# Kernel optimization log

Hardware: AMD Instinct MI355X
Metric: run time of the kernel (lower is better)

Reference implementation:

```python
import jax, jax.numpy as jnp
import numpy as np

P_SCALAR = 40.0
NEG_INF = -1e9


def setup_inputs() -> dict:
    key = jax.random.key(0)
    ks = jax.random.split(key, 6)
    B, Dk, Dv, T, H, W = 2, 128, 512, 2, 64, 64
    qkey = jax.random.normal(ks[0], (B, Dk, H, W), dtype=jnp.float32)
    qval = jax.random.normal(ks[1], (B, Dv, H, W), dtype=jnp.float32)
    mkey = jax.random.normal(ks[2], (B, Dk, T, H, W), dtype=jnp.float32)
    mval = jax.random.normal(ks[3], (B, Dv, T, H, W), dtype=jnp.float32)
    qmask = jax.random.bernoulli(ks[4], 0.5, (B, 1, H, W))
    mmask = jax.random.bernoulli(ks[5], 0.5, (B, 1, T, H, W))
    return {"qkey": qkey, "qval": qval, "qmask": qmask,
            "mkey": mkey, "mval": mval, "mmask": mmask}


def reference(qkey, qval, qmask, mkey, mval, mmask):
    # Faithful vectorized version of maskRead: for each batch, attention from
    # masked query pixels over masked memory pixels, scatter back into zeros.
    # Boolean-gather + softmax over gathered rows == full softmax with masked
    # logits set to -inf (rows outside mmask get zero probability).
    B, Dk, H, W = qkey.shape
    Dv = qval.shape[1]
    qk = qkey.reshape(B, Dk, H * W)            # [B, Dk, Nq]
    mk = mkey.reshape(B, Dk, -1)               # [B, Dk, Nm]
    mv = mval.reshape(B, Dv, -1)               # [B, Dv, Nm]
    qm = qmask.reshape(B, H * W)               # [B, Nq]
    mm = mmask.reshape(B, -1)                  # [B, Nm]

    # p[b, m, q] = <mk[b,:,m], qk[b,:,q]> * p_scalar, softmax over m
    p = jnp.einsum('bdm,bdq->bmq', mk, qk) * P_SCALAR
    p = jnp.where(mm[:, :, None], p, NEG_INF)
    p = jax.nn.softmax(p, axis=1)              # [B, Nm, Nq]

    read = jnp.einsum('bvm,bmq->bvq', mv, p)   # [B, Dv, Nq]

    # zero out query pixels outside qmask; skip batches with empty masks
    valid = qm[:, None, :] & mm.any(axis=1)[:, None, None] & qm.any(axis=1)[:, None, None]
    qread = jnp.where(valid, read, 0.0)
    return qread.reshape(B, Dv, H, W)
```

## Files before the change

### kernel.cpp

```cpp
#include <hip/hip_runtime.h>
#include <hip/hip_fp16.h>

#define NQ 4096
#define NM 8192
#define DK 128
#define DV 512
#define BATCH 2
#define NT (NM / 64)
#define KTS 8192
#define VTILE 16384

typedef __attribute__((ext_vector_type(8))) short short8;
typedef __attribute__((ext_vector_type(4))) float f32x4;
typedef unsigned short ushort_t;

#define MF(A_, B_, C_) __builtin_amdgcn_mfma_f32_16x16x32_bf16(A_, B_, C_, 0, 0, 0)

static __device__ __forceinline__ unsigned short f2bf(float x) {
    union { float f; unsigned int u; } c; c.f = x;
    unsigned int u = c.u;
    return (unsigned short)((u + 0x7FFFu + ((u >> 16) & 1u)) >> 16);
}
static __device__ __forceinline__ float bf2f(unsigned short h) {
    union { unsigned int u; float f; } c; c.u = ((unsigned int)h) << 16;
    return c.f;
}
static __device__ __forceinline__ ushort_t f2h(float x) {
    __half h = __float2half(x);
    return *(ushort_t*)&h;
}
static __device__ __forceinline__ float h2f(ushort_t u) {
    __half h = *(__half*)&u;
    return __half2float(h);
}

static __device__ __forceinline__ size_t vaddr(int b, int pos, int dv) {
    const int mt = pos >> 6, m64 = pos & 63;
    const int dvh = dv >> 8, rr = dv & 255;
    return (((size_t)(b * NT + mt) * 2 + dvh) * VTILE)
         + (rr >> 6) * 4096 + ((rr >> 4) & 3) * 1024
         + (m64 >> 5) * 512
         + ((((m64 >> 4) & 1) * 2 + ((m64 >> 3) & 1)) * 128)
         + (rr & 15) * 8 + (m64 & 7);
}

#define LOADK(AH, AL, itn_) do {                                              \
    const size_t ktb_ = kbase + (size_t)(itn_) * KTS;                         \
    _Pragma("unroll")                                                         \
    for (int ks_ = 0; ks_ < 4; ++ks_) {                                       \
        AH[ks_] = *(const short8*)(kh0 + ktb_ + ks_ * 512);                   \
        AL[ks_] = *(const short8*)(kl0 + ktb_ + ks_ * 512);                   \
    }                                                                         \
} while (0)

__global__ __launch_bounds__(1024) void scan_kernel(
    const int* __restrict__ qmask, const int* __restrict__ mmask,
    int* __restrict__ cidx, int* __restrict__ cpos,
    int* __restrict__ cnts, int* __restrict__ qflags) {
    const int b = blockIdx.x;
    const int t = threadIdx.x;
    const int lane = t & 63;
    const int w = t >> 6;
    __shared__ int wsum[16];
    __shared__ int qsh;

    const int* mp = mmask + b * NM;
    const int base = t * 8;
    int val[8];
#pragma unroll
    for (int i = 0; i < 8; ++i) val[i] = (mp[base + i] != 0);
    int c0 = 0;
#pragma unroll
    for (int i = 0; i < 8; ++i) c0 += val[i];

    int c = c0;
#pragma unroll
    for (int off = 1; off < 64; off <<= 1) {
        int n = __shfl_up(c, off, 64);
        if (lane >= off) c += n;
    }
    if (lane == 63) wsum[w] = c;
    if (t == 0) qsh = 0;
    __syncthreads();
    if (t == 0) {
        int s = 0;
#pragma unroll
        for (int i = 0; i < 16; ++i) { s += wsum[i]; wsum[i] = s; }
    }
    __syncthreads();
    const int wbase = (w == 0) ? 0 : wsum[w - 1];
    int run = wbase + (c - c0);
#pragma unroll
    for (int i = 0; i < 8; ++i) {
        int m = base + i;
        cpos[b * NM + m] = run;
        if (val[i]) { cidx[b * NM + run] = m; ++run; }
    }

    int qa = 0;
    for (int i = t; i < NQ; i += 1024) qa |= (qmask[b * NQ + i] != 0);
    if (qa) atomicOr(&qsh, 1);
    __syncthreads();
    if (t == 0) { cnts[b] = wsum[15]; qflags[b] = qsh; }
}

__global__ __launch_bounds__(256) void prep_qk_kernel(
    const float* __restrict__ qkey, const float* __restrict__ mkey,
    const int* __restrict__ mmask, const int* __restrict__ cpos,
    ushort_t* __restrict__ Qhi, ushort_t* __restrict__ Qlo,
    ushort_t* __restrict__ Khi, ushort_t* __restrict__ Klo) {
    __shared__ float t32[32][33];
    const int g = blockIdx.x;

    if (g < 1024) {
        const int bx = g & 127, by = (g >> 7) & 3, b = g >> 9;
        const int d0 = by * 32, n0 = bx * 32;
        for (int l = threadIdx.x; l < 1024; l += 256) {
            int r = l >> 5, c = l & 31;
            t32[r][c] = qkey[((size_t)b * DK + d0 + r) * NQ + n0 + c];
        }
        __syncthreads();
        for (int l = threadIdx.x; l < 1024; l += 256) {
            int r = l >> 5, c = l & 31;
            float f = t32[c][r];
            unsigned short h = f2bf(f);
            unsigned short lw = f2bf(f - bf2f(h));
            size_t off = ((size_t)b * NQ + n0 + r) * DK + d0 + c;
            Qhi[off] = h;
            Qlo[off] = lw;
        }
        return;
    }
    const int h0 = g - 1024;
    const int bx = h0 & 255, by = (h0 >> 8) & 3, b = h0 >> 10;
    const int d0 = by * 32, n0 = bx * 32;
    for (int l = threadIdx.x; l < 1024; l += 256) {
        int r = l >> 5, c = l & 31;
        t32[r][c] = mkey[((size_t)b * DK + d0 + r) * NM + n0 + c];
    }
    __syncthreads();
    for (int l = threadIdx.x; l < 1024; l += 256) {
        int r = l >> 5, c = l & 31;
        int m = n0 + r;
        if (mmask[b * NM + m] != 0) {
            int pos = cpos[b * NM + m];
            float f = t32[c][r];
            unsigned short hh = f2bf(f);
            unsigned short lw = f2bf(f - bf2f(hh));
            int d = d0 + c;
            size_t off = ((size_t)(b * NT + (pos >> 6))) * KTS
                       + ((pos >> 4) & 3) * 2048 + (d >> 5) * 512
                       + ((d >> 3) & 3) * 128 + (pos & 15) * 8 + (d & 7);
            Khi[off] = hh;
            Klo[off] = lw;
        }
    }
}

__global__ __launch_bounds__(256) void prep_v_kernel(
    const float* __restrict__ src, const int* __restrict__ mmask,
    const int* __restrict__ cpos, const int* __restrict__ cnts,
    ushort_t* __restrict__ dst) {
    const int b = blockIdx.z;
    const int dv0 = blockIdx.x * 8;
    if (blockIdx.y == 8) {
        const int cnt = cnts[b];
        const int pend = ((cnt + 63) >> 6) * 64;
        const int dv = dv0 + (threadIdx.x >> 5);
        for (int p = cnt + (threadIdx.x & 31); p < pend; p += 32)
            dst[vaddr(b, p, dv)] = 0;
        return;
    }
    const int m = blockIdx.y * 1024 + threadIdx.x * 4;
    const int4 mm = *(const int4*)(mmask + b * NM + m);
    const int4 cp = *(const int4*)(cpos + b * NM + m);
#pragma unroll
    for (int i = 0; i < 8; ++i) {
        const int dv = dv0 + i;
        const float4 v = *(const float4*)(src + ((size_t)b * DV + dv) * NM + m);
        if (mm.x) dst[vaddr(b, cp.x, dv)] = f2bf(v.x);
        if (mm.y) dst[vaddr(b, cp.y, dv)] = f2bf(v.y);
        if (mm.z) dst[vaddr(b, cp.z, dv)] = f2bf(v.z);
        if (mm.w) dst[vaddr(b, cp.w, dv)] = f2bf(v.w);
    }
}

__global__ __launch_bounds__(256, 3) void stats_kernel(
    const ushort_t* __restrict__ Qhi, const ushort_t* __restrict__ Khi,
    const int* __restrict__ cnts, float* __restrict__ mpart) {
    const int t = threadIdx.x;
    const int lane = t & 63;
    const int w = t >> 6;
    const int quad = lane >> 4;
    const int col = lane & 15;
    const int bid = blockIdx.x;
    const int part = bid & 3;
    const int b = (bid >> 2) & 1;
    const int qb = (bid >> 3) * 64;

    const int cnt = cnts[b];
    const int nit = (cnt + 63) >> 6;
    const int it0 = (nit * part) >> 2;
    const int it1 = (nit * (part + 1)) >> 2;

    __shared__ float red_m[4][64];

    short8 qfh[4][4];
    {
        const ushort_t* qhp = Qhi + ((size_t)b * NQ + qb) * DK;
#pragma unroll
        for (int qt = 0; qt < 4; ++qt)
#pragma unroll
            for (int ks = 0; ks < 4; ++ks)
                qfh[qt][ks] = *(const short8*)(qhp + (size_t)(qt * 16 + col) * DK + ks * 32 + quad * 8);
    }

    const f32x4 zero4 = {0.f, 0.f, 0.f, 0.f};
    float mloc[4] = {-3.0e38f, -3.0e38f, -3.0e38f, -3.0e38f};
    const ushort_t* kh0 = Khi + w * 2048 + lane * 8;
    const size_t kbase = (size_t)(b * NT) * KTS;

#define LOADKH(A_, itn_) do {                                                 \
    const size_t ktb_ = kbase + (size_t)(itn_) * KTS;                         \
    _Pragma("unroll")                                                         \
    for (int ks_ = 0; ks_ < 4; ++ks_)                                         \
        A_[ks_] = *(const short8*)(kh0 + ktb_ + ks_ * 512);                   \
} while (0)

#define STPH(CK, NK, it_, itn_) do {                                          \
    LOADKH(NK, itn_);                                                         \
    f32x4 aS[4];                                                              \
    _Pragma("unroll")                                                         \
    for (int qt = 0; qt < 4; ++qt) aS[qt] = zero4;                            \
    _Pragma("unroll")                                                         \
    for (int ks = 0; ks < 4; ++ks)                                            \
        _Pragma("unroll")                                                     \
        for (int qt = 0; qt < 4; ++qt)                                        \
            aS[qt] = MF(CK[ks], qfh[qt][ks], aS[qt]);                         \
    const int mrow_ = (it_) * 64 + w * 16 + quad * 4;                         \
    _Pragma("unroll")                                                         \
    for (int r = 0; r < 4; ++r) {                                             \
        if (mrow_ + r < cnt) {                                                \
            _Pragma("unroll")                                                 \
            for (int qt = 0; qt < 4; ++qt)                                    \
                mloc[qt] = fmaxf(mloc[qt], aS[qt][r] * 40.0f);                \
        }                                                                     \
    }                                                                         \
} while (0)

    short8 kA[4], kB[4];
    int it = it0;
    if (it < it1) {
        LOADKH(kA, it);
        int itn;
        while (true) {
            itn = (it + 1 < it1) ? it + 1 : it;
            STPH(kA, kB, it, itn);
            if (++it >= it1) break;
            itn = (it + 1 < it1) ? it + 1 : it;
            STPH(kB, kA, it, itn);
            if (++it >= it1) break;
        }
    }
#undef STPH
#undef LOADKH

#pragma unroll
    for (int qt = 0; qt < 4; ++qt) {
        float m = mloc[qt];
        m = fmaxf(m, __shfl_xor(m, 16, 64));
        m = fmaxf(m, __shfl_xor(m, 32, 64));
        if (lane < 16) red_m[w][qt * 16 + col] = m;
    }
    __syncthreads();
    if (t < 64) {
        float M = -3.0e38f;
#pragma unroll
        for (int ww = 0; ww < 4; ++ww) M = fmaxf(M, red_m[ww][t]);
        mpart[((size_t)(b * 4 + part)) * NQ + qb + t] = M;
    }
}

__global__ __launch_bounds__(256, 3) void pv_kernel(
    const ushort_t* __restrict__ Qhi, const ushort_t* __restrict__ Qlo,
    const ushort_t* __restrict__ Khi, const ushort_t* __restrict__ Klo,
    const ushort_t* __restrict__ Vimg, const int* __restrict__ cnts,
    const float* __restrict__ mpart, ushort_t* __restrict__ out0,
    ushort_t* __restrict__ out1, ushort_t* __restrict__ out2,
    float* __restrict__ lsum) {
    const int t = threadIdx.x;
    const int lane = t & 63;
    const int w = t >> 6;
    const int quad = lane >> 4;
    const int col = lane & 15;
    const int bid = blockIdx.x;
    const int b = bid & 1;
    const int dvh = (bid >> 1) & 1;
    const int r3 = bid >> 2;
    const int chunk = r3 % 3;
    const int qb = (r3 / 3) * 64;

    const int cnt = cnts[b];
    const int nit = (cnt + 63) >> 6;
    const int it0 = (nit * chunk) / 3;
    const int it1 = (nit * (chunk + 1)) / 3;

    __shared__ __align__(16) ushort_t Q_s[2][4][4][512];
    __shared__ __align__(16) ushort_t P_s[2][64][68];

    float gm[4];
#pragma unroll
    for (int qt = 0; qt < 4; ++qt) {
        float M = -3.0e38f;
#pragma unroll
        for (int c = 0; c < 4; ++c)
            M = fmaxf(M, mpart[((size_t)(b * 4 + c)) * NQ + qb + qt * 16 + col]);
        gm[qt] = M + 8.0f;
    }

    {
        const int r = t >> 2, ks4 = t & 3;
        const int qt_ = r >> 4, col_ = r & 15;
        const ushort_t* qhp = Qhi + ((size_t)b * NQ + qb + r) * DK + ks4 * 32;
        const ushort_t* qlp = Qlo + ((size_t)b * NQ + qb + r) * DK + ks4 * 32;
#pragma unroll
        for (int qd = 0; qd < 4; ++qd) {
            *(short8*)&Q_s[0][qt_][ks4][qd * 128 + col_ * 8] = *(const short8*)(qhp + qd * 8);
            *(short8*)&Q_s[1][qt_][ks4][qd * 128 + col_ * 8] = *(const short8*)(qlp + qd * 8);
        }
    }
    __syncthreads();

    const ushort_t* kh0 = Khi + w * 2048 + lane * 8;
    const ushort_t* kl0 = Klo + w * 2048 + lane * 8;
    const size_t kbase = (size_t)(b * NT) * KTS;
    const ushort_t* vl0 = Vimg + ((size_t)(b * NT) * 2 + dvh) * VTILE
                        + w * 4096 + lane * 8;

    const f32x4 zero4 = {0.f, 0.f, 0.f, 0.f};
    const short8 vones = {(short)0x3F80, (short)0x3F80, (short)0x3F80,
                          (short)0x3F80, (short)0x3F80, (short)0x3F80,
                          (short)0x3F80, (short)0x3F80};
    const bool doL = (dvh == 0) && (w == 0);
    f32x4 accO[4][4];
#pragma unroll
    for (int vt = 0; vt < 4; ++vt)
#pragma unroll
        for (int qt = 0; qt < 4; ++qt) accO[vt][qt] = zero4;
    f32x4 accL[4];
#pragma unroll
    for (int qt = 0; qt < 4; ++qt) accL[qt] = zero4;

    for (int it = it0; it < it1; ++it) {
        const int pb = (it - it0) & 1;
        short8 kh[4], kl[4];
        LOADK(kh, kl, it);
        f32x4 aS[4];
#pragma unroll
        for (int qt = 0; qt < 4; ++qt) aS[qt] = zero4;
        __builtin_amdgcn_s_setprio(1);
#pragma unroll
        for (int qt = 0; qt < 4; ++qt) {
#pragma unroll
            for (int ks = 0; ks < 4; ++ks) {
                const short8 qh = *(const short8*)&Q_s[0][qt][ks][lane * 8];
                const short8 ql = *(const short8*)&Q_s[1][qt][ks][lane * 8];
                aS[qt] = MF(kh[ks], qh, aS[qt]);
                aS[qt] = MF(kh[ks], ql, aS[qt]);
                aS[qt] = MF(kl[ks], qh, aS[qt]);
            }
        }
        __builtin_amdgcn_s_setprio(0);
        const ushort_t* vp = vl0 + (size_t)it * (2 * VTILE);
        short8 vf[4][2];
#pragma unroll
        for (int vt = 0; vt < 4; ++vt) {
            vf[vt][0] = *(const short8*)(vp + vt * 1024);
            vf[vt][1] = *(const short8*)(vp + vt * 1024 + 512);
        }
        const int mrow = it * 64 + w * 16 + quad * 4;
#pragma unroll
        for (int qt = 0; qt < 4; ++qt) {
            float p[4];
#pragma unroll
            for (int r = 0; r < 4; ++r)
                p[r] = (mrow + r < cnt) ? __expf(aS[qt][r] * 40.0f - gm[qt]) : 0.0f;
            ushort4 pk;
            pk.x = f2bf(p[0]); pk.y = f2bf(p[1]);
            pk.z = f2bf(p[2]); pk.w = f2bf(p[3]);
            *(ushort4*)&P_s[pb][qt * 16 + col][w * 16 + quad * 4] = pk;
        }
        asm volatile("s_waitcnt lgkmcnt(0)" ::: "memory");
        __builtin_amdgcn_s_barrier();
        __builtin_amdgcn_sched_barrier(0);
        __builtin_amdgcn_s_setprio(1);
#pragma unroll
        for (int k2 = 0; k2 < 2; ++k2) {
            short8 pq[4];
#pragma unroll
            for (int qt = 0; qt < 4; ++qt)
                pq[qt] = *(const short8*)&P_s[pb][qt * 16 + col][k2 * 32 + quad * 8];
#pragma unroll
            for (int vt = 0; vt < 4; ++vt)
#pragma unroll
                for (int qt = 0; qt < 4; ++qt)
                    accO[vt][qt] = MF(vf[vt][k2], pq[qt], accO[vt][qt]);
            if (doL) {
#pragma unroll
                for (int qt = 0; qt < 4; ++qt)
                    accL[qt] = MF(vones, pq[qt], accL[qt]);
            }
        }
        __builtin_amdgcn_s_setprio(0);
    }

    ushort_t* pbase = (chunk == 0) ? out0 : ((chunk == 1) ? out1 : out2);
#pragma unroll
    for (int qt = 0; qt < 4; ++qt) {
        const int q = qb + qt * 16 + col;
#pragma unroll
        for (int vt = 0; vt < 4; ++vt)
#pragma unroll
            for (int r = 0; r < 4; ++r) {
                int dv = dvh * 256 + w * 64 + vt * 16 + quad * 4 + r;
                pbase[((size_t)b * DV + dv) * NQ + q] = f2h(accO[vt][qt][r]);
            }
    }
    if (doL && lane < 16) {
#pragma unroll
        for (int qt = 0; qt < 4; ++qt)
            lsum[((size_t)(b * 3 + chunk)) * NQ + qb + qt * 16 + col] = accL[qt][0];
    }
}

__global__ __launch_bounds__(256) void combine_kernel(
    const ushort_t* __restrict__ p0, const ushort_t* __restrict__ p1,
    const ushort_t* __restrict__ p2, const float* __restrict__ lsum,
    const int* __restrict__ cnts, const int* __restrict__ qflags,
    const int* __restrict__ qmask, float* __restrict__ out) {
    const size_t i = ((size_t)blockIdx.x * 256 + threadIdx.x) * 4;
    const int b = (int)(i >> 21);
    const int q = (int)(i & (NQ - 1));
    ushort4 a4 = *(const ushort4*)(p0 + i);
    ushort4 c4 = *(const ushort4*)(p1 + i);
    ushort4 d4 = *(const ushort4*)(p2 + i);
    f32x4 l0 = *(const f32x4*)(lsum + (size_t)(b * 3) * NQ + q);
    f32x4 l1 = *(const f32x4*)(lsum + (size_t)(b * 3 + 1) * NQ + q);
    f32x4 l2 = *(const f32x4*)(lsum + (size_t)(b * 3 + 2) * NQ + q);
    const int4 qm = *(const int4*)(qmask + b * NQ + q);
    const bool bv = (qflags[b] != 0) && (cnts[b] > 0);
    f32x4 r;
    float lv;
    lv = l0[0] + l1[0] + l2[0];
    r[0] = (bv && qm.x && lv > 0.f) ? (h2f(a4.x) + h2f(c4.x) + h2f(d4.x)) / lv : 0.f;
    lv = l0[1] + l1[1] + l2[1];
    r[1] = (bv && qm.y && lv > 0.f) ? (h2f(a4.y) + h2f(c4.y) + h2f(d4.y)) / lv : 0.f;
    lv = l0[2] + l1[2] + l2[2];
    r[2] = (bv && qm.z && lv > 0.f) ? (h2f(a4.z) + h2f(c4.z) + h2f(d4.z)) / lv : 0.f;
    lv = l0[3] + l1[3] + l2[3];
    r[3] = (bv && qm.w && lv > 0.f) ? (h2f(a4.w) + h2f(c4.w) + h2f(d4.w)) / lv : 0.f;
    *(f32x4*)(out + i) = r;
}

extern "C" void kernel_launch(void* const* d_in, const int* in_sizes, int n_in,
                              void* d_out, int out_size, void* d_ws, size_t ws_size,
                              hipStream_t stream) {
    const float* qkey  = (const float*)d_in[0];
    const int*   qmask = (const int*)d_in[2];
    const float* mkey  = (const float*)d_in[3];
    const float* mval  = (const float*)d_in[4];
    const int*   mmask = (const int*)d_in[5];
    float* out = (float*)d_out;

    char* ws = (char*)d_ws;
    size_t off = 0;
    const size_t QS  = (size_t)BATCH * NQ * DK * 2;
    const size_t KS2 = (size_t)BATCH * NM * DK * 2;
    const size_t VS  = (size_t)BATCH * NT * 2 * VTILE * 2;
    const size_t OS2 = (size_t)BATCH * DV * NQ * 2;
    ushort_t* Qhi = (ushort_t*)(ws + off); off += QS;
    ushort_t* Qlo = (ushort_t*)(ws + off); off += QS;
    ushort_t* Khi = (ushort_t*)(ws + off); off += KS2;
    ushort_t* Klo = (ushort_t*)(ws + off); off += KS2;
    ushort_t* Vc  = (ushort_t*)(ws + off); off += VS;
    ushort_t* part0 = (ushort_t*)(ws + off); off += OS2;
    ushort_t* part1 = (ushort_t*)(ws + off); off += OS2;
    ushort_t* part2 = (ushort_t*)(ws + off); off += OS2;
    float* mpart  = (float*)(ws + off); off += (size_t)BATCH * 4 * NQ * 4;
    float* lsum   = (float*)(ws + off); off += (size_t)BATCH * 3 * NQ * 4;
    int* cidx     = (int*)(ws + off); off += (size_t)BATCH * NM * 4;
    int* cpos     = (int*)(ws + off); off += (size_t)BATCH * NM * 4;
    int* cnts     = (int*)(ws + off); off += 64;
    int* qflags   = (int*)(ws + off); off += 64;

    scan_kernel<<<BATCH, 1024, 0, stream>>>(qmask, mmask, cidx, cpos, cnts, qflags);

    prep_qk_kernel<<<3072, 256, 0, stream>>>(
        qkey, mkey, mmask, cpos, Qhi, Qlo, Khi, Klo);

    dim3 gv(DV / 8, 9, BATCH);
    prep_v_kernel<<<gv, 256, 0, stream>>>(mval, mmask, cpos, cnts, Vc);

    stats_kernel<<<(NQ / 64) * 8, 256, 0, stream>>>(Qhi, Khi, cnts, mpart);

    pv_kernel<<<(NQ / 64) * 12, 256, 0, stream>>>(
        Qhi, Qlo, Khi, Klo, Vc, cnts, mpart, part0, part1, part2, lsum);

    combine_kernel<<<(int)((size_t)BATCH * DV * NQ / 1024), 256, 0, stream>>>(
        part0, part1, part2, lsum, cnts, qflags, qmask, out);
}
```

Measured before the change: 221.6 us.

## Software-pipeline PV loop, compute row sums on VALU, fuse prep kernels

Restructures the pv_kernel main loop into a two-stage software pipeline. The QK^T MFMAs for tile it overlap the PV MFMAs for tile it-1, and K and V fragments are double-buffered in registers and prefetched one iteration ahead. Softmax row sums are now accumulated from the bf16-rounded P values on the VALU with a shuffle and LDS reduction, which removes the extra MFMA against a ones vector. The QK and V prep kernels are merged into one launch to cut launch overhead. Occupancy is lowered to 2 blocks per SM to make room for the extra registers, so latency hiding between waves may suffer.

After: 386.9 us. 74.6% more time.

```diff
diff --git a/kernel.cpp b/kernel.cpp
--- a/kernel.cpp
+++ b/kernel.cpp
@@ -50,6 +50,15 @@
     for (int ks_ = 0; ks_ < 4; ++ks_) {                                       \
         AH[ks_] = *(const short8*)(kh0 + ktb_ + ks_ * 512);                   \
         AL[ks_] = *(const short8*)(kl0 + ktb_ + ks_ * 512);                   \
+    }                                                                         \
+} while (0)
+
+#define LOADV(VB_, it_) do {                                                  \
+    const ushort_t* vp_ = vl0 + (size_t)(it_) * (2 * VTILE);                  \
+    _Pragma("unroll")                                                         \
+    for (int vt_ = 0; vt_ < 4; ++vt_) {                                       \
+        VB_[vt_][0] = *(const short8*)(vp_ + vt_ * 1024);                     \
+        VB_[vt_][1] = *(const short8*)(vp_ + vt_ * 1024 + 512);               \
     }                                                                         \
 } while (0)
 
@@ -104,11 +113,13 @@
     if (t == 0) { cnts[b] = wsum[15]; qflags[b] = qsh; }
 }
 
-__global__ __launch_bounds__(256) void prep_qk_kernel(
+__global__ __launch_bounds__(256) void prep_all_kernel(
     const float* __restrict__ qkey, const float* __restrict__ mkey,
-    const int* __restrict__ mmask, const int* __restrict__ cpos,
+    const float* __restrict__ mval, const int* __restrict__ mmask,
+    const int* __restrict__ cpos, const int* __restrict__ cnts,
     ushort_t* __restrict__ Qhi, ushort_t* __restrict__ Qlo,
-    ushort_t* __restrict__ Khi, ushort_t* __restrict__ Klo) {
+    ushort_t* __restrict__ Khi, ushort_t* __restrict__ Klo,
+    ushort_t* __restrict__ Vc) {
     __shared__ float t32[32][33];
     const int g = blockIdx.x;
 
@@ -131,57 +142,57 @@
         }
         return;
     }
-    const int h0 = g - 1024;
-    const int bx = h0 & 255, by = (h0 >> 8) & 3, b = h0 >> 10;
-    const int d0 = by * 32, n0 = bx * 32;
-    for (int l = threadIdx.x; l < 1024; l += 256) {
-        int r = l >> 5, c = l & 31;
-        t32[r][c] = mkey[((size_t)b * DK + d0 + r) * NM + n0 + c];
-    }
-    __syncthreads();
-    for (int l = threadIdx.x; l < 1024; l += 256) {
-        int r = l >> 5, c = l & 31;
-        int m = n0 + r;
-        if (mmask[b * NM + m] != 0) {
-            int pos = cpos[b * NM + m];
-            float f = t32[c][r];
-            unsigned short hh = f2bf(f);
-            unsigned short lw = f2bf(f - bf2f(hh));
-            int d = d0 + c;
-            size_t off = ((size_t)(b * NT + (pos >> 6))) * KTS
-                       + ((pos >> 4) & 3) * 2048 + (d >> 5) * 512
-                       + ((d >> 3) & 3) * 128 + (pos & 15) * 8 + (d & 7);
-            Khi[off] = hh;
-            Klo[off] = lw;
-        }
-    }
-}
-
-__global__ __launch_bounds__(256) void prep_v_kernel(
-    const float* __restrict__ src, const int* __restrict__ mmask,
-    const int* __restrict__ cpos, const int* __restrict__ cnts,
-    ushort_t* __restrict__ dst) {
-    const int b = blockIdx.z;
-    const int dv0 = blockIdx.x * 8;
-    if (blockIdx.y == 8) {
+    if (g < 3072) {
+        const int h0 = g - 1024;
+        const int bx = h0 & 255, by = (h0 >> 8) & 3, b = h0 >> 10;
+        const int d0 = by * 32, n0 = bx * 32;
+        for (int l = threadIdx.x; l < 1024; l += 256) {
+            int r = l >> 5, c = l & 31;
+            t32[r][c] = mkey[((size_t)b * DK + d0 + r) * NM + n0 + c];
+        }
+        __syncthreads();
+        for (int l = threadIdx.x; l < 1024; l += 256) {
+            int r = l >> 5, c = l & 31;
+            int m = n0 + r;
+            if (mmask[b * NM + m] != 0) {
+                int pos = cpos[b * NM + m];
+                float f = t32[c][r];
+                unsigned short hh = f2bf(f);
+                unsigned short lw = f2bf(f - bf2f(hh));
+                int d = d0 + c;
+                size_t off = ((size_t)(b * NT + (pos >> 6))) * KTS
+                           + ((pos >> 4) & 3) * 2048 + (d >> 5) * 512
+                           + ((d >> 3) & 3) * 128 + (pos & 15) * 8 + (d & 7);
+                Khi[off] = hh;
+                Klo[off] = lw;
+            }
+        }
+        return;
+    }
+    const int h0 = g - 3072;
+    const int bx = h0 & 63;
+    const int by = (h0 >> 6) % 9;
+    const int b = h0 / 576;
+    const int dv0 = bx * 8;
+    if (by == 8) {
         const int cnt = cnts[b];
         const int pend = ((cnt + 63) >> 6) * 64;
         const int dv = dv0 + (threadIdx.x >> 5);
         for (int p = cnt + (threadIdx.x & 31); p < pend; p += 32)
-            dst[vaddr(b, p, dv)] = 0;
+            Vc[vaddr(b, p, dv)] = 0;
         return;
     }
-    const int m = blockIdx.y * 1024 + threadIdx.x * 4;
+    const int m = by * 1024 + threadIdx.x * 4;
     const int4 mm = *(const int4*)(mmask + b * NM + m);
     const int4 cp = *(const int4*)(cpos + b * NM + m);
 #pragma unroll
     for (int i = 0; i < 8; ++i) {
         const int dv = dv0 + i;
-        const float4 v = *(const float4*)(src + ((size_t)b * DV + dv) * NM + m);
-        if (mm.x) dst[vaddr(b, cp.x, dv)] = f2bf(v.x);
-        if (mm.y) dst[vaddr(b, cp.y, dv)] = f2bf(v.y);
-        if (mm.z) dst[vaddr(b, cp.z, dv)] = f2bf(v.z);
-        if (mm.w) dst[vaddr(b, cp.w, dv)] = f2bf(v.w);
+        const float4 v = *(const float4*)(mval + ((size_t)b * DV + dv) * NM + m);
+        if (mm.x) Vc[vaddr(b, cp.x, dv)] = f2bf(v.x);
+        if (mm.y) Vc[vaddr(b, cp.y, dv)] = f2bf(v.y);
+        if (mm.z) Vc[vaddr(b, cp.z, dv)] = f2bf(v.z);
+        if (mm.w) Vc[vaddr(b, cp.w, dv)] = f2bf(v.w);
     }
 }
 
@@ -281,7 +292,7 @@
     }
 }
 
-__global__ __launch_bounds__(256, 3) void pv_kernel(
+__global__ __launch_bounds__(256, 2) void pv_kernel(
     const ushort_t* __restrict__ Qhi, const ushort_t* __restrict__ Qlo,
     const ushort_t* __restrict__ Khi, const ushort_t* __restrict__ Klo,
     const ushort_t* __restrict__ Vimg, const int* __restrict__ cnts,
@@ -307,6 +318,7 @@
 
     __shared__ __align__(16) ushort_t Q_s[2][4][4][512];
     __shared__ __align__(16) ushort_t P_s[2][64][68];
+    __shared__ float red_l[4][64];
 
     float gm[4];
 #pragma unroll
@@ -338,81 +350,110 @@
                         + w * 4096 + lane * 8;
 
     const f32x4 zero4 = {0.f, 0.f, 0.f, 0.f};
-    const short8 vones = {(short)0x3F80, (short)0x3F80, (short)0x3F80,
-                          (short)0x3F80, (short)0x3F80, (short)0x3F80,
-                          (short)0x3F80, (short)0x3F80};
-    const bool doL = (dvh == 0) && (w == 0);
     f32x4 accO[4][4];
 #pragma unroll
     for (int vt = 0; vt < 4; ++vt)
 #pragma unroll
         for (int qt = 0; qt < 4; ++qt) accO[vt][qt] = zero4;
-    f32x4 accL[4];
-#pragma unroll
-    for (int qt = 0; qt < 4; ++qt) accL[qt] = zero4;
-
-    for (int it = it0; it < it1; ++it) {
-        const int pb = (it - it0) & 1;
-        short8 kh[4], kl[4];
-        LOADK(kh, kl, it);
-        f32x4 aS[4];
-#pragma unroll
-        for (int qt = 0; qt < 4; ++qt) aS[qt] = zero4;
-        __builtin_amdgcn_s_setprio(1);
-#pragma unroll
-        for (int qt = 0; qt < 4; ++qt) {
-#pragma unroll
-            for (int ks = 0; ks < 4; ++ks) {
-                const short8 qh = *(const short8*)&Q_s[0][qt][ks][lane * 8];
-                const short8 ql = *(const short8*)&Q_s[1][qt][ks][lane * 8];
-                aS[qt] = MF(kh[ks], qh, aS[qt]);
-                aS[qt] = MF(kh[ks], ql, aS[qt]);
-                aS[qt] = MF(kl[ks], qh, aS[qt]);
-            }
-        }
-        __builtin_amdgcn_s_setprio(0);
-        const ushort_t* vp = vl0 + (size_t)it * (2 * VTILE);
-        short8 vf[4][2];
-#pragma unroll
-        for (int vt = 0; vt < 4; ++vt) {
-            vf[vt][0] = *(const short8*)(vp + vt * 1024);
-            vf[vt][1] = *(const short8*)(vp + vt * 1024 + 512);
-        }
-        const int mrow = it * 64 + w * 16 + quad * 4;
-#pragma unroll
-        for (int qt = 0; qt < 4; ++qt) {
-            float p[4];
-#pragma unroll
-            for (int r = 0; r < 4; ++r)
-                p[r] = (mrow + r < cnt) ? __expf(aS[qt][r] * 40.0f - gm[qt]) : 0.0f;
-            ushort4 pk;
-            pk.x = f2bf(p[0]); pk.y = f2bf(p[1]);
-            pk.z = f2bf(p[2]); pk.w = f2bf(p[3]);
-            *(ushort4*)&P_s[pb][qt * 16 + col][w * 16 + quad * 4] = pk;
+    float lacc[4] = {0.f, 0.f, 0.f, 0.f};
+
+#define QKBLK(KH_, KL_) do {                                                  \
+    __builtin_amdgcn_s_setprio(1);                                            \
+    _Pragma("unroll")                                                         \
+    for (int qt = 0; qt < 4; ++qt) {                                          \
+        _Pragma("unroll")                                                     \
+        for (int ks = 0; ks < 4; ++ks) {                                      \
+            const short8 qh = *(const short8*)&Q_s[0][qt][ks][lane * 8];      \
+            const short8 ql = *(const short8*)&Q_s[1][qt][ks][lane * 8];      \
+            aS[qt] = MF(KH_[ks], qh, aS[qt]);                                 \
+            aS[qt] = MF(KH_[ks], ql, aS[qt]);                                 \
+            aS[qt] = MF(KL_[ks], qh, aS[qt]);                                 \
+        }                                                                     \
+    }                                                                         \
+    __builtin_amdgcn_s_setprio(0);                                            \
+} while (0)
+
+#define PSTORE(PW_, it_) do {                                                 \
+    const int mrow_ = (it_) * 64 + w * 16 + quad * 4;                         \
+    _Pragma("unroll")                                                         \
+    for (int qt = 0; qt < 4; ++qt) {                                          \
+        float p_[4];                                                          \
+        _Pragma("unroll")                                                     \
+        for (int r = 0; r < 4; ++r)                                           \
+            p_[r] = (mrow_ + r < cnt) ? __expf(aS[qt][r] * 40.0f - gm[qt]) : 0.0f; \
+        ushort4 pk_;                                                          \
+        pk_.x = f2bf(p_[0]); pk_.y = f2bf(p_[1]);                             \
+        pk_.z = f2bf(p_[2]); pk_.w = f2bf(p_[3]);                             \
+        *(ushort4*)&P_s[PW_][qt * 16 + col][w * 16 + quad * 4] = pk_;         \
+        lacc[qt] += bf2f(pk_.x) + bf2f(pk_.y) + bf2f(pk_.z) + bf2f(pk_.w);    \
+    }                                                                         \
+} while (0)
+
+#define PVBLK(VP_, PBR_) do {                                                 \
+    short8 pq_[2][4];                                                         \
+    _Pragma("unroll")                                                         \
+    for (int k2 = 0; k2 < 2; ++k2)                                            \
+        _Pragma("unroll")                                                     \
+        for (int qt = 0; qt < 4; ++qt)                                        \
+            pq_[k2][qt] = *(const short8*)&P_s[PBR_][qt * 16 + col][k2 * 32 + quad * 8]; \
+    __builtin_amdgcn_s_setprio(1);                                            \
+    _Pragma("unroll")                                                         \
+    for (int k2 = 0; k2 < 2; ++k2)                                            \
+        _Pragma("unroll")                                                     \
+        for (int vt = 0; vt < 4; ++vt)                                        \
+            _Pragma("unroll")                                                 \
+            for (int qt = 0; qt < 4; ++qt)                                    \
+                accO[vt][qt] = MF(VP_[vt][k2], pq_[k2][qt], accO[vt][qt]);    \
+    __builtin_amdgcn_s_setprio(0);                                            \
+} while (0)
+
+#define PHASE(VP, VN, KC, KN, PBR, PBW, it_) do {                             \
+    LOADV(VN, it_);                                                           \
+    f32x4 aS[4];                                                              \
+    _Pragma("unroll")                                                         \
+    for (int qt = 0; qt < 4; ++qt) aS[qt] = zero4;                            \
+    QKBLK(KC##h, KC##l);                                                      \
+    { int itn_ = ((it_) + 1 < it1) ? (it_) + 1 : (it_);                       \
+      LOADK(KN##h, KN##l, itn_); }                                            \
+    PVBLK(VP, PBR);                                                           \
+    PSTORE(PBW, it_);                                                         \
+    asm volatile("s_waitcnt lgkmcnt(0)" ::: "memory");                        \
+    __builtin_amdgcn_s_barrier();                                             \
+    __builtin_amdgcn_sched_barrier(0);                                        \
+} while (0)
+
+    short8 kAh[4], kAl[4], kBh[4], kBl[4];
+    short8 vA[4][2], vB[4][2];
+    int it = it0;
+    if (it < it1) {
+        LOADV(vA, it);
+        LOADK(kAh, kAl, it);
+        {
+            f32x4 aS[4];
+#pragma unroll
+            for (int qt = 0; qt < 4; ++qt) aS[qt] = zero4;
+            QKBLK(kAh, kAl);
+            { int itn_ = (it + 1 < it1) ? it + 1 : it; LOADK(kBh, kBl, itn_); }
+            PSTORE(0, it);
         }
         asm volatile("s_waitcnt lgkmcnt(0)" ::: "memory");
         __builtin_amdgcn_s_barrier();
         __builtin_amdgcn_sched_barrier(0);
-        __builtin_amdgcn_s_setprio(1);
-#pragma unroll
-        for (int k2 = 0; k2 < 2; ++k2) {
-            short8 pq[4];
-#pragma unroll
-            for (int qt = 0; qt < 4; ++qt)
-                pq[qt] = *(const short8*)&P_s[pb][qt * 16 + col][k2 * 32 + quad * 8];
-#pragma unroll
-            for (int vt = 0; vt < 4; ++vt)
-#pragma unroll
-                for (int qt = 0; qt < 4; ++qt)
-                    accO[vt][qt] = MF(vf[vt][k2], pq[qt], accO[vt][qt]);
-            if (doL) {
-#pragma unroll
-                for (int qt = 0; qt < 4; ++qt)
-                    accL[qt] = MF(vones, pq[qt], accL[qt]);
-            }
-        }
-        __builtin_amdgcn_s_setprio(0);
-    }
+        ++it;
+        while (it < it1) {
+            PHASE(vA, vB, kB, kA, 0, 1, it);
+            if (++it >= it1) break;
+            PHASE(vB, vA, kA, kB, 1, 0, it);
+            if (++it >= it1) break;
+        }
+        const int lastp = (it1 - 1 - it0) & 1;
+        if (lastp) PVBLK(vB, 1);
+        else       PVBLK(vA, 0);
+    }
+#undef PHASE
+#undef PVBLK
+#undef PSTORE
+#undef QKBLK
 
     ushort_t* pbase = (chunk == 0) ? out0 : ((chunk == 1) ? out1 : out2);
 #pragma unroll
@@ -426,10 +467,19 @@
                 pbase[((size_t)b * DV + dv) * NQ + q] = f2h(accO[vt][qt][r]);
             }
     }
-    if (doL && lane < 16) {
-#pragma unroll
-        for (int qt = 0; qt < 4; ++qt)
-            lsum[((size_t)(b * 3 + chunk)) * NQ + qb + qt * 16 + col] = accL[qt][0];
+#pragma unroll
+    for (int qt = 0; qt < 4; ++qt) {
+        float v = lacc[qt];
+        v += __shfl_xor(v, 16, 64);
+        v += __shfl_xor(v, 32, 64);
+        if (lane < 16) red_l[w][qt * 16 + col] = v;
+    }
+    __syncthreads();
+    if (dvh == 0 && t < 64) {
+        float L = 0.f;
+#pragma unroll
+        for (int ww = 0; ww < 4; ++ww) L += red_l[ww][t];
+        lsum[((size_t)(b * 3 + chunk)) * NQ + qb + t] = L;
     }
 }
 
@@ -495,11 +545,8 @@
 
     scan_kernel<<<BATCH, 1024, 0, stream>>>(qmask, mmask, cidx, cpos, cnts, qflags);
 
-    prep_qk_kernel<<<3072, 256, 0, stream>>>(
-        qkey, mkey, mmask, cpos, Qhi, Qlo, Khi, Klo);
-
-    dim3 gv(DV / 8, 9, BATCH);
-    prep_v_kernel<<<gv, 256, 0, stream>>>(mval, mmask, cpos, cnts, Vc);
+    prep_all_kernel<<<4224, 256, 0, stream>>>(
+        qkey, mkey, mval, mmask, cpos, cnts, Qhi, Qlo, Khi, Klo, Vc);
 
     stats_kernel<<<(NQ / 64) * 8, 256, 0, stream>>>(Qhi, Khi, cnts, mpart);
 
```

## Fuse V compaction into stats kernel and switch to gather-based vectorized V packing

Applied to the files above, without the earlier changes.

Merges the V preparation and the row-max stats pass into one launch. The first 2048 blocks pack compacted V tiles and the remaining 512 blocks compute the stats, so the two independent stages can overlap and one launch is saved. V packing now gathers through the compacted index list and writes two 16-byte vectors per thread, instead of scattering 2-byte stores through cpos. It also skips tiles beyond the compacted count. The cost is a random-access gather on the mval rows, and the V blocks now run under the stats kernel's launch bounds.

Result: slower. 236.0 us (+6.5%).

```diff
diff --git a/kernel.cpp b/kernel.cpp
--- a/kernel.cpp
+++ b/kernel.cpp
@@ -32,16 +32,6 @@
 static __device__ __forceinline__ float h2f(ushort_t u) {
     __half h = *(__half*)&u;
     return __half2float(h);
-}
-
-static __device__ __forceinline__ size_t vaddr(int b, int pos, int dv) {
-    const int mt = pos >> 6, m64 = pos & 63;
-    const int dvh = dv >> 8, rr = dv & 255;
-    return (((size_t)(b * NT + mt) * 2 + dvh) * VTILE)
-         + (rr >> 6) * 4096 + ((rr >> 4) & 3) * 1024
-         + (m64 >> 5) * 512
-         + ((((m64 >> 4) & 1) * 2 + ((m64 >> 3) & 1)) * 128)
-         + (rr & 15) * 8 + (m64 & 7);
 }
 
 #define LOADK(AH, AL, itn_) do {                                              \
@@ -157,53 +147,58 @@
     }
 }
 
-__global__ __launch_bounds__(256) void prep_v_kernel(
-    const float* __restrict__ src, const int* __restrict__ mmask,
-    const int* __restrict__ cpos, const int* __restrict__ cnts,
-    ushort_t* __restrict__ dst) {
-    const int b = blockIdx.z;
-    const int dv0 = blockIdx.x * 8;
-    if (blockIdx.y == 8) {
+__global__ __launch_bounds__(256, 3) void prep_v_stats_kernel(
+    const float* __restrict__ mval, const int* __restrict__ cidx,
+    const int* __restrict__ cnts, ushort_t* __restrict__ Vc,
+    const ushort_t* __restrict__ Qhi, const ushort_t* __restrict__ Khi,
+    float* __restrict__ mpart) {
+    const int g = blockIdx.x;
+    __shared__ float red_m[4][64];
+
+    if (g < 2048) {
+        const int mt = g & 127;
+        const int dvb = (g >> 7) & 7;
+        const int b = g >> 10;
         const int cnt = cnts[b];
         const int pend = ((cnt + 63) >> 6) * 64;
-        const int dv = dv0 + (threadIdx.x >> 5);
-        for (int p = cnt + (threadIdx.x & 31); p < pend; p += 32)
-            dst[vaddr(b, p, dv)] = 0;
+        if (mt * 64 >= pend) return;
+        const int tr = threadIdx.x >> 2;
+        const int part = threadIdx.x & 3;
+        const int dv = dvb * 64 + tr;
+        const int dvh = dv >> 8, rr = dv & 255;
+        const int wq = rr >> 6, vt = (rr >> 4) & 3, cl = rr & 15;
+        const int ks2 = part >> 1, quad0 = (part & 1) * 2;
+
+        const float* row = mval + ((size_t)b * DV + dv) * NM;
+        const int* cx = cidx + b * NM + mt * 64 + part * 16;
+        ushort_t o[16];
+#pragma unroll
+        for (int i = 0; i < 16; ++i) {
+            int m = mt * 64 + part * 16 + i;
+            int idx = (m < cnt) ? cx[i] : 0;
+            o[i] = (m < cnt) ? f2bf(row[idx]) : (ushort_t)0;
+        }
+        ushort_t* dp = Vc + (((size_t)(b * NT + mt)) * 2 + dvh) * VTILE
+                     + wq * 4096 + vt * 1024 + ks2 * 512 + quad0 * 128 + cl * 8;
+        *(short8*)dp = *(short8*)&o[0];
+        *(short8*)(dp + 128) = *(short8*)&o[8];
         return;
     }
-    const int m = blockIdx.y * 1024 + threadIdx.x * 4;
-    const int4 mm = *(const int4*)(mmask + b * NM + m);
-    const int4 cp = *(const int4*)(cpos + b * NM + m);
-#pragma unroll
-    for (int i = 0; i < 8; ++i) {
-        const int dv = dv0 + i;
-        const float4 v = *(const float4*)(src + ((size_t)b * DV + dv) * NM + m);
-        if (mm.x) dst[vaddr(b, cp.x, dv)] = f2bf(v.x);
-        if (mm.y) dst[vaddr(b, cp.y, dv)] = f2bf(v.y);
-        if (mm.z) dst[vaddr(b, cp.z, dv)] = f2bf(v.z);
-        if (mm.w) dst[vaddr(b, cp.w, dv)] = f2bf(v.w);
-    }
-}
-
-__global__ __launch_bounds__(256, 3) void stats_kernel(
-    const ushort_t* __restrict__ Qhi, const ushort_t* __restrict__ Khi,
-    const int* __restrict__ cnts, float* __restrict__ mpart) {
+
+    const int sid = g - 2048;
     const int t = threadIdx.x;
     const int lane = t & 63;
     const int w = t >> 6;
     const int quad = lane >> 4;
     const int col = lane & 15;
-    const int bid = blockIdx.x;
-    const int part = bid & 3;
-    const int b = (bid >> 2) & 1;
-    const int qb = (bid >> 3) * 64;
+    const int part = sid & 3;
+    const int b = (sid >> 2) & 1;
+    const int qb = (sid >> 3) * 64;
 
     const int cnt = cnts[b];
     const int nit = (cnt + 63) >> 6;
     const int it0 = (nit * part) >> 2;
     const int it1 = (nit * (part + 1)) >> 2;
-
-    __shared__ float red_m[4][64];
 
     short8 qfh[4][4];
     {
@@ -498,10 +493,8 @@
     prep_qk_kernel<<<3072, 256, 0, stream>>>(
         qkey, mkey, mmask, cpos, Qhi, Qlo, Khi, Klo);
 
-    dim3 gv(DV / 8, 9, BATCH);
-    prep_v_kernel<<<gv, 256, 0, stream>>>(mval, mmask, cpos, cnts, Vc);
-
-    stats_kernel<<<(NQ / 64) * 8, 256, 0, stream>>>(Qhi, Khi, cnts, mpart);
+    prep_v_stats_kernel<<<2560, 256, 0, stream>>>(
+        mval, cidx, cnts, Vc, Qhi, Khi, mpart);
 
     pv_kernel<<<(NQ / 64) * 12, 256, 0, stream>>>(
         Qhi, Qlo, Khi, Klo, Vc, cnts, mpart, part0, part1, part2, lsum);
```

## Fuse split-K combine into pv_kernel via last-block atomic counter

Applied to the files above, without the earlier changes.

Removes the separate combine kernel launch. Each pv block bumps a per-(batch, query-tile) atomic counter after writing its partial outputs and row sums. The sixth block to arrive (3 chunks x 2 Dv halves) merges the three fp16 partials, normalizes by the summed row sums and writes the final output. This saves a kernel launch and lets the combine overlap with the tail of pv work, but puts the combine on a few last-arriving blocks and adds threadfence and atomic traffic. The counters are reset inside scan_kernel.

Measured after the change: 381.2 us. 1.72x slower.

```diff
diff --git a/kernel.cpp b/kernel.cpp
--- a/kernel.cpp
+++ b/kernel.cpp
@@ -56,13 +56,16 @@
 __global__ __launch_bounds__(1024) void scan_kernel(
     const int* __restrict__ qmask, const int* __restrict__ mmask,
     int* __restrict__ cidx, int* __restrict__ cpos,
-    int* __restrict__ cnts, int* __restrict__ qflags) {
+    int* __restrict__ cnts, int* __restrict__ qflags,
+    int* __restrict__ done) {
     const int b = blockIdx.x;
     const int t = threadIdx.x;
     const int lane = t & 63;
     const int w = t >> 6;
     __shared__ int wsum[16];
     __shared__ int qsh;
+
+    if (t < 64) done[b * 64 + t] = 0;
 
     const int* mp = mmask + b * NM;
     const int base = t * 8;
@@ -285,9 +288,11 @@
     const ushort_t* __restrict__ Qhi, const ushort_t* __restrict__ Qlo,
     const ushort_t* __restrict__ Khi, const ushort_t* __restrict__ Klo,
     const ushort_t* __restrict__ Vimg, const int* __restrict__ cnts,
-    const float* __restrict__ mpart, ushort_t* __restrict__ out0,
-    ushort_t* __restrict__ out1, ushort_t* __restrict__ out2,
-    float* __restrict__ lsum) {
+    const float* __restrict__ mpart, ushort_t* __restrict__ part0,
+    ushort_t* __restrict__ part1, ushort_t* __restrict__ part2,
+    float* __restrict__ lsum, const int* __restrict__ qflags,
+    const int* __restrict__ qmask, int* __restrict__ done,
+    float* __restrict__ out) {
     const int t = threadIdx.x;
     const int lane = t & 63;
     const int w = t >> 6;
@@ -307,6 +312,7 @@
 
     __shared__ __align__(16) ushort_t Q_s[2][4][4][512];
     __shared__ __align__(16) ushort_t P_s[2][64][68];
+    __shared__ int lastflag;
 
     float gm[4];
 #pragma unroll
@@ -414,7 +420,7 @@
         __builtin_amdgcn_s_setprio(0);
     }
 
-    ushort_t* pbase = (chunk == 0) ? out0 : ((chunk == 1) ? out1 : out2);
+    ushort_t* pbase = (chunk == 0) ? part0 : ((chunk == 1) ? part1 : part2);
 #pragma unroll
     for (int qt = 0; qt < 4; ++qt) {
         const int q = qb + qt * 16 + col;
@@ -431,35 +437,38 @@
         for (int qt = 0; qt < 4; ++qt)
             lsum[((size_t)(b * 3 + chunk)) * NQ + qb + qt * 16 + col] = accL[qt][0];
     }
-}
-
-__global__ __launch_bounds__(256) void combine_kernel(
-    const ushort_t* __restrict__ p0, const ushort_t* __restrict__ p1,
-    const ushort_t* __restrict__ p2, const float* __restrict__ lsum,
-    const int* __restrict__ cnts, const int* __restrict__ qflags,
-    const int* __restrict__ qmask, float* __restrict__ out) {
-    const size_t i = ((size_t)blockIdx.x * 256 + threadIdx.x) * 4;
-    const int b = (int)(i >> 21);
-    const int q = (int)(i & (NQ - 1));
-    ushort4 a4 = *(const ushort4*)(p0 + i);
-    ushort4 c4 = *(const ushort4*)(p1 + i);
-    ushort4 d4 = *(const ushort4*)(p2 + i);
-    f32x4 l0 = *(const f32x4*)(lsum + (size_t)(b * 3) * NQ + q);
-    f32x4 l1 = *(const f32x4*)(lsum + (size_t)(b * 3 + 1) * NQ + q);
-    f32x4 l2 = *(const f32x4*)(lsum + (size_t)(b * 3 + 2) * NQ + q);
-    const int4 qm = *(const int4*)(qmask + b * NQ + q);
-    const bool bv = (qflags[b] != 0) && (cnts[b] > 0);
-    f32x4 r;
+
+    __threadfence();
+    if (t == 0)
+        lastflag = (atomicAdd(&done[b * 64 + (qb >> 6)], 1) == 5);
+    __syncthreads();
+    if (lastflag == 0) return;
+    __threadfence();
+
+    const bool bv = (qflags[b] != 0) && (cnt > 0);
+    const int q0 = qb + (t & 15) * 4;
+    f32x4 l0 = *(const f32x4*)(lsum + (size_t)(b * 3) * NQ + q0);
+    f32x4 l1 = *(const f32x4*)(lsum + (size_t)(b * 3 + 1) * NQ + q0);
+    f32x4 l2 = *(const f32x4*)(lsum + (size_t)(b * 3 + 2) * NQ + q0);
+    const int4 qm = *(const int4*)(qmask + b * NQ + q0);
+    f32x4 rinv;
     float lv;
-    lv = l0[0] + l1[0] + l2[0];
-    r[0] = (bv && qm.x && lv > 0.f) ? (h2f(a4.x) + h2f(c4.x) + h2f(d4.x)) / lv : 0.f;
-    lv = l0[1] + l1[1] + l2[1];
-    r[1] = (bv && qm.y && lv > 0.f) ? (h2f(a4.y) + h2f(c4.y) + h2f(d4.y)) / lv : 0.f;
-    lv = l0[2] + l1[2] + l2[2];
-    r[2] = (bv && qm.z && lv > 0.f) ? (h2f(a4.z) + h2f(c4.z) + h2f(d4.z)) / lv : 0.f;
-    lv = l0[3] + l1[3] + l2[3];
-    r[3] = (bv && qm.w && lv > 0.f) ? (h2f(a4.w) + h2f(c4.w) + h2f(d4.w)) / lv : 0.f;
-    *(f32x4*)(out + i) = r;
+    lv = l0[0] + l1[0] + l2[0]; rinv[0] = (bv && qm.x && lv > 0.f) ? 1.f / lv : 0.f;
+    lv = l0[1] + l1[1] + l2[1]; rinv[1] = (bv && qm.y && lv > 0.f) ? 1.f / lv : 0.f;
+    lv = l0[2] + l1[2] + l2[2]; rinv[2] = (bv && qm.z && lv > 0.f) ? 1.f / lv : 0.f;
+    lv = l0[3] + l1[3] + l2[3]; rinv[3] = (bv && qm.w && lv > 0.f) ? 1.f / lv : 0.f;
+    for (int dv = (t >> 4); dv < DV; dv += 16) {
+        const size_t o = ((size_t)b * DV + dv) * NQ + q0;
+        ushort4 a4 = *(const ushort4*)(part0 + o);
+        ushort4 c4 = *(const ushort4*)(part1 + o);
+        ushort4 d4 = *(const ushort4*)(part2 + o);
+        f32x4 r;
+        r[0] = (h2f(a4.x) + h2f(c4.x) + h2f(d4.x)) * rinv[0];
+        r[1] = (h2f(a4.y) + h2f(c4.y) + h2f(d4.y)) * rinv[1];
+        r[2] = (h2f(a4.z) + h2f(c4.z) + h2f(d4.z)) * rinv[2];
+        r[3] = (h2f(a4.w) + h2f(c4.w) + h2f(d4.w)) * rinv[3];
+        *(f32x4*)(out + o) = r;
+    }
 }
 
 extern "C" void kernel_launch(void* const* d_in, const int* in_sizes, int n_in,
@@ -492,8 +501,10 @@
     int* cpos     = (int*)(ws + off); off += (size_t)BATCH * NM * 4;
     int* cnts     = (int*)(ws + off); off += 64;
     int* qflags   = (int*)(ws + off); off += 64;
-
-    scan_kernel<<<BATCH, 1024, 0, stream>>>(qmask, mmask, cidx, cpos, cnts, qflags);
+    int* done     = (int*)(ws + off); off += 512;
+
+    scan_kernel<<<BATCH, 1024, 0, stream>>>(
+        qmask, mmask, cidx, cpos, cnts, qflags, done);
 
     prep_qk_kernel<<<3072, 256, 0, stream>>>(
         qkey, mkey, mmask, cpos, Qhi, Qlo, Khi, Klo);
@@ -504,8 +515,6 @@
     stats_kernel<<<(NQ / 64) * 8, 256, 0, stream>>>(Qhi, Khi, cnts, mpart);
 
     pv_kernel<<<(NQ / 64) * 12, 256, 0, stream>>>(
-        Qhi, Qlo, Khi, Klo, Vc, cnts, mpart, part0, part1, part2, lsum);
-
-    combine_kernel<<<(int)((size_t)BATCH * DV * NQ / 1024), 256, 0, stream>>>(
-        part0, part1, part2, lsum, cnts, qflags, qmask, out);
-}
+        Qhi, Qlo, Khi, Klo, Vc, cnts, mpart, part0, part1, part2, lsum,
+        qflags, qmask, done, out);
+}
```
